# Kernel tuning notes

Hardware: AMD Instinct MI355X
Metric: run time of the kernel (lower is better)

## Reference

```python
import jax, jax.numpy as jnp
import numpy as np
from jax import lax

T, R, W, F_CWT, E, H, HG, NC, K = 16, 200, 50, 32, 128, 256, 256, 2, 20


def _make_wavelets():
    t = np.linspace(-1.0, 1.0, W)
    w0 = 6.0
    freqs = np.linspace(1.0, W / 2.0, F_CWT)
    wr = np.zeros((F_CWT, 1, W), np.float32)
    wi = np.zeros((F_CWT, 1, W), np.float32)
    for i, s in enumerate(freqs):
        norm = s ** (-0.5) * np.pi ** (-0.25)
        ts = t / s
        psi = norm * np.exp(1j * w0 * ts) * np.exp(-0.5 * ts ** 2)
        wr[i, 0] = psi.real.astype(np.float32)
        wi[i, 0] = psi.imag.astype(np.float32)
    return jnp.asarray(wr), jnp.asarray(wi)


def setup_inputs() -> dict:
    key = jax.random.key(0)
    ks = jax.random.split(key, 20)
    wr, wi = _make_wavelets()
    s = 0.05
    inp = {
        "time_windows": jax.random.normal(ks[0], (T, R, W), jnp.float32),
        "wav_real": wr, "wav_imag": wi,
        "conv1_w": jax.random.normal(ks[1], (16, 1, 3, 3), jnp.float32) * s,
        "conv1_b": jnp.zeros((16,), jnp.float32),
        "bn1_g": jnp.ones((16,), jnp.float32), "bn1_b": jnp.zeros((16,), jnp.float32),
        "conv2_w": jax.random.normal(ks[2], (32, 16, 3, 3), jnp.float32) * s,
        "conv2_b": jnp.zeros((32,), jnp.float32),
        "bn2_g": jnp.ones((32,), jnp.float32), "bn2_b": jnp.zeros((32,), jnp.float32),
        "fc_w": jax.random.normal(ks[3], (E, 32), jnp.float32) * s,
        "fc_b": jnp.zeros((E,), jnp.float32),
        "q_w": jax.random.normal(ks[4], (E, E), jnp.float32) * s,
        "q_b": jnp.zeros((E,), jnp.float32),
        "k_w": jax.random.normal(ks[5], (E, E), jnp.float32) * s,
        "k_b": jnp.zeros((E,), jnp.float32),
        "gcn1_w": jax.random.normal(ks[6], (E, H), jnp.float32) * s,
        "gcn1_b": jnp.zeros((H,), jnp.float32),
        "gcn2_w": jax.random.normal(ks[7], (H, H), jnp.float32) * s,
        "gcn2_b": jnp.zeros((H,), jnp.float32),
        "gru_wih": jax.random.normal(ks[8], (3 * HG, H), jnp.float32) * s,
        "gru_whh": jax.random.normal(ks[9], (3 * HG, HG), jnp.float32) * s,
        "gru_bih": jnp.zeros((3 * HG,), jnp.float32),
        "gru_bhh": jnp.zeros((3 * HG,), jnp.float32),
        "cls_w": jax.random.normal(ks[10], (NC, HG), jnp.float32) * s,
        "cls_b": jnp.zeros((NC,), jnp.float32),
    }
    return inp


def _conv_bn_relu_pool(x, w, b, g, beta):
    # conv2d k3 pad1, training-mode BN, relu, maxpool2 (floor)
    x = lax.conv_general_dilated(x, w, (1, 1), ((1, 1), (1, 1)),
                                 dimension_numbers=("NCHW", "OIHW", "NCHW"))
    x = x + b[None, :, None, None]
    mu = x.mean((0, 2, 3), keepdims=True)
    var = x.var((0, 2, 3), keepdims=True)
    x = (x - mu) * lax.rsqrt(var + 1e-5) * g[None, :, None, None] + beta[None, :, None, None]
    x = jax.nn.relu(x)
    return lax.reduce_window(x, -jnp.inf, lax.max, (1, 1, 2, 2), (1, 1, 2, 2), "VALID")


def _forward(time_windows, wav_real, wav_imag, conv1_w, conv1_b, bn1_g, bn1_b,
             conv2_w, conv2_b, bn2_g, bn2_b, fc_w, fc_b, q_w, q_b, k_w, k_b,
             gcn1_w, gcn1_b, gcn2_w, gcn2_b, gru_wih, gru_whh, gru_bih, gru_bhh,
             cls_w, cls_b):
    N = T * R
    x = time_windows.reshape(N, 1, W)
    pl = (W - 1) // 2
    pr = (W - 1) - pl  # torch padding='same' (extra on right)
    re = lax.conv_general_dilated(x, wav_real, (1,), [(pl, pr)],
                                  dimension_numbers=("NCH", "OIH", "NCH"))
    im = lax.conv_general_dilated(x, wav_imag, (1,), [(pl, pr)],
                                  dimension_numbers=("NCH", "OIH", "NCH"))
    scal = jnp.sqrt(re * re + im * im)              # [N, F_CWT, W]

    h = scal[:, None]                               # [N,1,F,W]
    h = _conv_bn_relu_pool(h, conv1_w, conv1_b, bn1_g, bn1_b)
    h = _conv_bn_relu_pool(h, conv2_w, conv2_b, bn2_g, bn2_b)
    pooled = h.mean((2, 3))                         # adaptive avg pool -> [N,32]
    emb = pooled @ fc_w.T + fc_b                    # [N,E]
    emb = emb.reshape(T, R, E)

    # sparse-attention graph generation (per window, vectorized over T)
    Q = emb @ q_w.T + q_b
    Kp = emb @ k_w.T + k_b
    attn = jnp.einsum("tre,tse->trs", Q, Kp) / (E ** 0.5)
    attn = jax.nn.leaky_relu(attn, 0.2)
    _, idx = lax.top_k(attn, K)                     # [T,R,K]
    mask = jnp.zeros_like(attn).at[
        jnp.arange(T)[:, None, None], jnp.arange(R)[None, :, None], idx].set(1.0)
    masked = attn * mask
    masked = jnp.where(masked == 0.0, -1e9, masked)
    adj = jax.nn.softmax(masked, axis=-1)           # [T,R,R] row-stochastic, topk-sparse

    # GCNConv x2 with edge weights (PyG gcn_norm: remaining self-loops weight 1,
    ii = jnp.arange(R)
    diag = adj[:, ii, ii]
    adj_sl = adj.at[:, ii, ii].set(jnp.where(diag == 0.0, 1.0, diag))
    Bm = jnp.swapaxes(adj_sl, 1, 2)
    deg = Bm.sum(-1)
    dinv = jnp.where(deg > 0, deg, 1.0) ** -0.5
    An = dinv[:, :, None] * Bm * dinv[:, None, :]   # [T,R,R]
    g = jax.nn.relu(jnp.einsum("trs,tsh->trh", An, emb @ gcn1_w) + gcn1_b)
    g = jax.nn.relu(jnp.einsum("trs,tsh->trh", An, g @ gcn2_w) + gcn2_b)
    g_emb = g.mean(1)                               # [T,H]

    # GRU over the T graph embeddings (batch 1, gate order r,z,n)
    def step(hprev, xt):
        gi = xt @ gru_wih.T + gru_bih
        gh = hprev @ gru_whh.T + gru_bhh
        ir, iz, inn = jnp.split(gi, 3)
        hr, hz, hn = jnp.split(gh, 3)
        r = jax.nn.sigmoid(ir + hr)
        z = jax.nn.sigmoid(iz + hz)
        n = jnp.tanh(inn + r * hn)
        return (1.0 - z) * n + z * hprev, None

    hT, _ = lax.scan(step, jnp.zeros((HG,), emb.dtype), g_emb)
    pred = (hT @ cls_w.T + cls_b)[None]             # [1,NC]

    edge_var = jnp.mean(jnp.var(adj, axis=0, ddof=1))
    avg_adj = adj.mean(0)[None]                     # [1,R,R]
    return pred, avg_adj, edge_var


def reference(time_windows, wav_real, wav_imag, conv1_w, conv1_b, bn1_g, bn1_b,
              conv2_w, conv2_b, bn2_g, bn2_b, fc_w, fc_b, q_w, q_b, k_w, k_b,
              gcn1_w, gcn1_b, gcn2_w, gcn2_b, gru_wih, gru_whh, gru_bih, gru_bhh,
              cls_w, cls_b):
    return _forward(time_windows, wav_real, wav_imag, conv1_w, conv1_b, bn1_g, bn1_b,
                    conv2_w, conv2_b, bn2_g, bn2_b, fc_w, fc_b, q_w, q_b, k_w, k_b,
                    gcn1_w, gcn1_b, gcn2_w, gcn2_b, gru_wih, gru_whh, gru_bih, gru_bhh,
                    cls_w, cls_b)
```

## Files before the change

### kernel.cpp

```cpp
#include <hip/hip_runtime.h>
#include <cfloat>
#include <cmath>

#define T_ 16
#define R_ 200
#define W_ 50
#define FCWT 32
#define E_ 128
#define K_ 20
#define N_ 3200
#define GRU_BLOCKS 6

__device__ __forceinline__ void waveReduce2(float& a, float& b) {
#pragma unroll
    for (int o = 32; o > 0; o >>= 1) {
        a += __shfl_down(a, o, 64);
        b += __shfl_down(b, o, 64);
    }
}

__global__ __launch_bounds__(256) void transpose_multi_kernel(const float* __restrict__ wih,
                                                              const float* __restrict__ whh,
                                                              const float* __restrict__ qw,
                                                              const float* __restrict__ kw,
                                                              const float* __restrict__ fcw,
                                                              float* __restrict__ wihT,
                                                              float* __restrict__ whhT,
                                                              float* __restrict__ qwT,
                                                              float* __restrict__ kwT,
                                                              float* __restrict__ fcwT) {
    int b = blockIdx.x, tid = threadIdx.x;
    if (b < 768) {
        int gid = b * 256 + tid; int k = gid / 768, j = gid % 768;
        wihT[gid] = wih[j * 256 + k];
    } else if (b < 1536) {
        int gid = (b - 768) * 256 + tid; int k = gid / 768, j = gid % 768;
        whhT[gid] = whh[j * 256 + k];
    } else if (b < 1600) {
        int gid = (b - 1536) * 256 + tid; int k = gid >> 7, e = gid & 127;
        qwT[gid] = qw[e * 128 + k];
    } else if (b < 1664) {
        int gid = (b - 1600) * 256 + tid; int k = gid >> 7, e = gid & 127;
        kwT[gid] = kw[e * 128 + k];
    } else {
        int gid = (b - 1664) * 256 + tid; int c = gid >> 7, e = gid & 127;
        fcwT[gid] = fcw[e * 32 + c];
    }
}

__global__ __launch_bounds__(256) void cwt_conv1_stats_kernel(const float* __restrict__ x,
                                                              const float* __restrict__ wr,
                                                              const float* __restrict__ wi,
                                                              const float* __restrict__ w1,
                                                              const float* __restrict__ b1,
                                                              float* __restrict__ scalP,
                                                              double* __restrict__ psum,
                                                              double* __restrict__ psq) {
    int n = blockIdx.x, tid = threadIdx.x;
    __shared__ float sxp[112];
    __shared__ float swr[FCWT * W_];
    __shared__ float swi[FCWT * W_];
    __shared__ float P1[34 * 52];
    __shared__ float ls[256], lq[256];
    if (tid < 112) sxp[tid] = (tid >= 24 && tid < 74) ? x[n * 50 + (tid - 24)] : 0.f;
    for (int idx = tid; idx < FCWT * W_; idx += 256) { swr[idx] = wr[idx]; swi[idx] = wi[idx]; }
    for (int idx = tid; idx < 34 * 52; idx += 256) P1[idx] = 0.f;
    __syncthreads();
    {
        int f = tid >> 3, cg = tid & 7, i0 = cg * 7;
        float xw[7], ar[7], ai[7];
#pragma unroll
        for (int d = 0; d < 7; ++d) { xw[d] = sxp[i0 + d]; ar[d] = 0.f; ai[d] = 0.f; }
        const float* wrf = &swr[f * 50];
        const float* wif = &swi[f * 50];
        for (int j = 0; j < 50; ++j) {
            float wrv = wrf[j], wiv = wif[j];
#pragma unroll
            for (int d = 0; d < 7; ++d) { ar[d] += xw[d] * wrv; ai[d] += xw[d] * wiv; }
#pragma unroll
            for (int d = 0; d < 6; ++d) xw[d] = xw[d + 1];
            xw[6] = sxp[i0 + j + 7];
        }
#pragma unroll
        for (int d = 0; d < 7; ++d) {
            int i = i0 + d;
            if (i < 50) P1[(f + 1) * 52 + i + 1] = sqrtf(ar[d] * ar[d] + ai[d] * ai[d]);
        }
    }
    __syncthreads();
    for (int idx = tid; idx < 34 * 52; idx += 256) scalP[(size_t)n * 1768 + idx] = P1[idx];
    int c = tid & 15, pg = tid >> 4;
    float wv[9];
#pragma unroll
    for (int k = 0; k < 9; ++k) wv[k] = w1[c * 9 + k];
    float bias = b1[c];
    const float* r0p = &P1[(2 * pg + 0) * 52];
    const float* r1p = &P1[(2 * pg + 1) * 52];
    const float* r2p = &P1[(2 * pg + 2) * 52];
    const float* r3p = &P1[(2 * pg + 3) * 52];
    float c0[4], c1[4];
    c0[0] = r0p[0]; c0[1] = r1p[0]; c0[2] = r2p[0]; c0[3] = r3p[0];
    c1[0] = r0p[1]; c1[1] = r1p[1]; c1[2] = r2p[1]; c1[3] = r3p[1];
    float s = 0.f, q = 0.f;
    for (int xx = 0; xx < 50; ++xx) {
        float c2[4];
        c2[0] = r0p[xx + 2]; c2[1] = r1p[xx + 2]; c2[2] = r2p[xx + 2]; c2[3] = r3p[xx + 2];
        float v0 = bias + c0[0] * wv[0] + c1[0] * wv[1] + c2[0] * wv[2]
                        + c0[1] * wv[3] + c1[1] * wv[4] + c2[1] * wv[5]
                        + c0[2] * wv[6] + c1[2] * wv[7] + c2[2] * wv[8];
        float v1 = bias + c0[1] * wv[0] + c1[1] * wv[1] + c2[1] * wv[2]
                        + c0[2] * wv[3] + c1[2] * wv[4] + c2[2] * wv[5]
                        + c0[3] * wv[6] + c1[3] * wv[7] + c2[3] * wv[8];
        s += v0 + v1; q += v0 * v0 + v1 * v1;
#pragma unroll
        for (int rr = 0; rr < 4; ++rr) { c0[rr] = c1[rr]; c1[rr] = c2[rr]; }
    }
    ls[tid] = s; lq[tid] = q;
    __syncthreads();
    if (tid < 16) {
        float ss = 0.f, qq = 0.f;
        for (int g = 0; g < 16; ++g) { ss += ls[tid + 16 * g]; qq += lq[tid + 16 * g]; }
        psum[n * 16 + tid] = (double)ss;
        psq[n * 16 + tid] = (double)qq;
    }
}

__global__ __launch_bounds__(256) void bn_finalize_kernel(const double* __restrict__ psum,
                                                          const double* __restrict__ psq,
                                                          const float* __restrict__ g,
                                                          const float* __restrict__ beta,
                                                          float* __restrict__ scale,
                                                          float* __restrict__ shift,
                                                          int C, double inv_count) {
    int c = blockIdx.x, tid = threadIdx.x;
    double s = 0.0, q = 0.0;
    for (int n = tid; n < N_; n += 256) { s += psum[n * C + c]; q += psq[n * C + c]; }
#pragma unroll
    for (int o = 32; o > 0; o >>= 1) { s += __shfl_down(s, o, 64); q += __shfl_down(q, o, 64); }
    __shared__ double sa[4], sb[4];
    int lane = tid & 63, wid = tid >> 6;
    if (lane == 0) { sa[wid] = s; sb[wid] = q; }
    __syncthreads();
    if (tid == 0) {
        s = sa[0] + sa[1] + sa[2] + sa[3];
        q = sb[0] + sb[1] + sb[2] + sb[3];
        double mu = s * inv_count;
        double var = q * inv_count - mu * mu;
        double rstd = 1.0 / sqrt(var + 1e-5);
        double gg = (double)g[c];
        scale[c] = (float)(gg * rstd);
        shift[c] = (float)((double)beta[c] - mu * rstd * gg);
    }
}

__global__ __launch_bounds__(256) void conv1_norm_pool_kernel(const float* __restrict__ scalP,
                                                              const float* __restrict__ w1,
                                                              const float* __restrict__ b1,
                                                              const float* __restrict__ scale,
                                                              const float* __restrict__ shift,
                                                              float* __restrict__ pooled1) {
    int n = blockIdx.x, tid = threadIdx.x;
    __shared__ float P1[34 * 52];
    __shared__ float outb[6400];
    for (int idx = tid; idx < 34 * 52; idx += 256) P1[idx] = scalP[(size_t)n * 1768 + idx];
    __syncthreads();
    int c = tid & 15, py = tid >> 4;
    float wv[9];
#pragma unroll
    for (int k = 0; k < 9; ++k) wv[k] = w1[c * 9 + k];
    float bias = b1[c], sc = scale[c], sh = shift[c];
    const float* r0p = &P1[(2 * py + 0) * 52];
    const float* r1p = &P1[(2 * py + 1) * 52];
    const float* r2p = &P1[(2 * py + 2) * 52];
    const float* r3p = &P1[(2 * py + 3) * 52];
    float c0[4], c1[4];
    c0[0] = r0p[0]; c0[1] = r1p[0]; c0[2] = r2p[0]; c0[3] = r3p[0];
    c1[0] = r0p[1]; c1[1] = r1p[1]; c1[2] = r2p[1]; c1[3] = r3p[1];
    float pmax = -FLT_MAX;
    for (int xx = 0; xx < 50; ++xx) {
        float c2[4];
        c2[0] = r0p[xx + 2]; c2[1] = r1p[xx + 2]; c2[2] = r2p[xx + 2]; c2[3] = r3p[xx + 2];
        float v0 = bias + c0[0] * wv[0] + c1[0] * wv[1] + c2[0] * wv[2]
                        + c0[1] * wv[3] + c1[1] * wv[4] + c2[1] * wv[5]
                        + c0[2] * wv[6] + c1[2] * wv[7] + c2[2] * wv[8];
        float v1 = bias + c0[1] * wv[0] + c1[1] * wv[1] + c2[1] * wv[2]
                        + c0[2] * wv[3] + c1[2] * wv[4] + c2[2] * wv[5]
                        + c0[3] * wv[6] + c1[3] * wv[7] + c2[3] * wv[8];
        float m2 = fmaxf(v0 * sc + sh, v1 * sc + sh);
        if ((xx & 1) == 0) pmax = m2;
        else outb[(c * 16 + py) * 25 + (xx >> 1)] = fmaxf(fmaxf(pmax, m2), 0.f);
#pragma unroll
        for (int rr = 0; rr < 4; ++rr) { c0[rr] = c1[rr]; c1[rr] = c2[rr]; }
    }
    __syncthreads();
    const float4* ob4 = (const float4*)outb;
    float4* p4 = (float4*)(pooled1 + (size_t)n * 6400);
    for (int idx = tid; idx < 1600; idx += 256) p4[idx] = ob4[idx];
}

__global__ __launch_bounds__(256) void conv2_compute_kernel(const float* __restrict__ pooled1,
                                                            const float* __restrict__ w2,
                                                            const float* __restrict__ b2,
                                                            float* __restrict__ mm,
                                                            double* __restrict__ psum,
                                                            double* __restrict__ psq) {
    int n = blockIdx.x, tid = threadIdx.x;
    __shared__ float P2[16 * 18 * 28];
    __shared__ float swT[144 * 32];
    __shared__ float ls[256], lq[256];
    for (int idx = tid; idx < 16 * 18 * 28; idx += 256) {
        int ci = idx / 504, rem = idx % 504, yy = rem / 28, xx = rem % 28;
        float v = 0.f;
        if (yy >= 1 && yy <= 16 && xx >= 1 && xx <= 25)
            v = pooled1[((size_t)n * 16 + ci) * 400 + (yy - 1) * 25 + (xx - 1)];
        P2[idx] = v;
    }
    for (int idx = tid; idx < 4608; idx += 256) {
        int co = idx / 144, r = idx % 144;
        swT[r * 32 + co] = w2[idx];
    }
    __syncthreads();
    int co = tid & 31, pg = tid >> 5;
    float bias = b2[co];
    float acc0[25], acc1[25];
#pragma unroll
    for (int cv = 0; cv < 25; ++cv) { acc0[cv] = bias; acc1[cv] = bias; }
    for (int ci = 0; ci < 16; ++ci) {
        const float* wb = &swT[ci * 288 + co];
        float w[9];
#pragma unroll
        for (int k = 0; k < 9; ++k) w[k] = wb[k * 32];
        const float* base = &P2[ci * 504 + (2 * pg) * 28];
#pragma unroll
        for (int iy = 0; iy < 4; ++iy) {
            float r[28];
            const float4* rp = (const float4*)(base + iy * 28);
#pragma unroll
            for (int m = 0; m < 7; ++m) {
                float4 v4 = rp[m];
                r[4 * m] = v4.x; r[4 * m + 1] = v4.y; r[4 * m + 2] = v4.z; r[4 * m + 3] = v4.w;
            }
            if (iy < 3) {
                int kb = iy * 3;
#pragma unroll
                for (int cv = 0; cv < 25; ++cv)
                    acc0[cv] += r[cv] * w[kb] + r[cv + 1] * w[kb + 1] + r[cv + 2] * w[kb + 2];
            }
            if (iy >= 1) {
                int kb = (iy - 1) * 3;
#pragma unroll
                for (int cv = 0; cv < 25; ++cv)
                    acc1[cv] += r[cv] * w[kb] + r[cv + 1] * w[kb + 1] + r[cv + 2] * w[kb + 2];
            }
        }
    }
    float s = 0.f, q = 0.f;
#pragma unroll
    for (int cv = 0; cv < 25; ++cv) {
        s += acc0[cv] + acc1[cv];
        q += acc0[cv] * acc0[cv] + acc1[cv] * acc1[cv];
    }
#pragma unroll
    for (int pc = 0; pc < 12; ++pc) {
        float v00 = acc0[2 * pc], v01 = acc0[2 * pc + 1];
        float v10 = acc1[2 * pc], v11 = acc1[2 * pc + 1];
        float mx = fmaxf(fmaxf(v00, v01), fmaxf(v10, v11));
        int cell = pg * 12 + pc;
        mm[((size_t)n * 96 + cell) * 32 + co] = mx;
    }
    ls[tid] = s; lq[tid] = q;
    __syncthreads();
    if (tid < 32) {
        float ss = 0.f, qq = 0.f;
        for (int g2 = 0; g2 < 8; ++g2) { ss += ls[tid + 32 * g2]; qq += lq[tid + 32 * g2]; }
        psum[n * 32 + tid] = (double)ss;
        psq[n * 32 + tid] = (double)qq;
    }
}

__global__ __launch_bounds__(256) void pm_fc_qk_kernel(const float* __restrict__ mm,
                                                       const float* __restrict__ scale,
                                                       const float* __restrict__ shift,
                                                       const float* __restrict__ fcwT,
                                                       const float* __restrict__ fc_b,
                                                       const float* __restrict__ qwT,
                                                       const float* __restrict__ q_b,
                                                       const float* __restrict__ kwT,
                                                       const float* __restrict__ k_b,
                                                       float* __restrict__ emb,
                                                       float* __restrict__ Q,
                                                       float* __restrict__ Kp) {
    int n = blockIdx.x, tid = threadIdx.x;
    int co = tid & 31, grp = tid >> 5;
    __shared__ float red[256];
    __shared__ float pm_s[32];
    __shared__ float se[128];
    float sc = scale[co], sh = shift[co];
    float acc = 0.f;
    for (int j = 0; j < 12; ++j) {
        int cell = grp * 12 + j;
        float mx = mm[((size_t)n * 96 + cell) * 32 + co];
        acc += fmaxf(mx * sc + sh, 0.f);
    }
    red[tid] = acc;
    __syncthreads();
    if (tid < 32) {
        float t = 0.f;
        for (int g = 0; g < 8; ++g) t += red[co + 32 * g];
        pm_s[tid] = t * (1.f / 96.f);
    }
    __syncthreads();
    if (tid < 128) {
        float a = fc_b[tid];
        for (int c = 0; c < 32; ++c) a += pm_s[c] * fcwT[c * 128 + tid];
        se[tid] = a;
        emb[(size_t)n * 128 + tid] = a;
    }
    __syncthreads();
    {
        int e = tid & 127, half = tid >> 7;
        const float* w = half ? kwT : qwT;
        float b = half ? k_b[e] : q_b[e];
        float a = b;
        for (int k = 0; k < 128; ++k) a += se[k] * w[k * 128 + e];
        if (half) Kp[(size_t)n * 128 + e] = a;
        else      Q[(size_t)n * 128 + e] = a;
    }
}

__global__ __launch_bounds__(256) void attn_topk_kernel(const float* __restrict__ Q,
                                                        const float* __restrict__ Kp,
                                                        float* __restrict__ adj) {
    int r = blockIdx.x, t = blockIdx.y, tid = threadIdx.x;
    __shared__ float sq[128];
    __shared__ float sc[200];
    if (tid < 128) sq[tid] = Q[(size_t)(t * 200 + r) * 128 + tid];
    __syncthreads();
    if (tid < 200) {
        const float4* kp4 = (const float4*)(Kp + (size_t)(t * 200 + tid) * 128);
        float acc = 0.f;
#pragma unroll 8
        for (int e4 = 0; e4 < 32; ++e4) {
            float4 k4 = kp4[e4];
            acc += sq[e4 * 4 + 0] * k4.x + sq[e4 * 4 + 1] * k4.y +
                   sq[e4 * 4 + 2] * k4.z + sq[e4 * 4 + 3] * k4.w;
        }
        acc = acc / 11.313708498984761f;
        sc[tid] = (acc >= 0.f) ? acc : 0.2f * acc;
    }
    __syncthreads();
    if (tid < 64) {
        int lane = tid;
        float v[4], w[4];
#pragma unroll
        for (int j = 0; j < 4; ++j) {
            int i = lane + 64 * j;
            float x = (i < 200) ? sc[i] : -FLT_MAX;
            v[j] = x; w[j] = x;
        }
        unsigned sel = 0;
        for (int it = 0; it < K_; ++it) {
            float best = -FLT_MAX; int bidx = 0x7fffffff;
#pragma unroll
            for (int j = 0; j < 4; ++j) {
                int i = lane + 64 * j;
                if (w[j] > best || (w[j] == best && i < bidx)) { best = w[j]; bidx = i; }
            }
#pragma unroll
            for (int off = 32; off > 0; off >>= 1) {
                float ob = __shfl_down(best, off, 64);
                int oi = __shfl_down(bidx, off, 64);
                if (ob > best || (ob == best && oi < bidx)) { best = ob; bidx = oi; }
            }
            bidx = __shfl(bidx, 0, 64);
            if ((bidx & 63) == lane) { int j = bidx >> 6; w[j] = -FLT_MAX; sel |= (1u << j); }
        }
        float mv[4]; float m = -FLT_MAX;
#pragma unroll
        for (int j = 0; j < 4; ++j) {
            int i = lane + 64 * j;
            float x = -1e9f;
            if (i < 200 && ((sel >> j) & 1u)) x = (v[j] == 0.f) ? -1e9f : v[j];
            mv[j] = x; m = fmaxf(m, x);
        }
#pragma unroll
        for (int off = 32; off > 0; off >>= 1) m = fmaxf(m, __shfl_xor(m, off, 64));
        float s = 0.f; float e[4];
#pragma unroll
        for (int j = 0; j < 4; ++j) {
            int i = lane + 64 * j;
            e[j] = (i < 200) ? expf(mv[j] - m) : 0.f;
            s += e[j];
        }
#pragma unroll
        for (int off = 32; off > 0; off >>= 1) s += __shfl_xor(s, off, 64);
        float inv = 1.f / s;
        size_t rowo = (size_t)(t * 200 + r) * 200;
#pragma unroll
        for (int j = 0; j < 4; ++j) {
            int i = lane + 64 * j;
            if (i < 200) adj[rowo + i] = e[j] * inv;
        }
    }
}

__global__ __launch_bounds__(256) void deg_kernel(const float* __restrict__ adj,
                                                  float* __restrict__ dinv) {
    int t = blockIdx.x, tid = threadIdx.x;
    if (tid < 200) {
        float acc = 0.f;
        for (int s = 0; s < 200; ++s) {
            float v = adj[(size_t)(t * 200 + s) * 200 + tid];
            if (s == tid) v = (v == 0.f) ? 1.f : v;
            acc += v;
        }
        float d = (acc > 0.f) ? acc : 1.f;
        dinv[t * 200 + tid] = 1.f / sqrtf(d);
    }
}

__global__ __launch_bounds__(256) void an_tile_kernel(const float* __restrict__ adj,
                                                      const float* __restrict__ dinv,
                                                      float* __restrict__ An) {
    int t = blockIdx.y;
    int tr = blockIdx.x >> 2, tc = blockIdx.x & 3;
    int r0 = tr * 50, s0 = tc * 50;
    int tid = threadIdx.x;
    __shared__ float Tt[50 * 51];
    __shared__ float dr[50], ds[50];
    for (int idx = tid; idx < 2500; idx += 256) {
        int a = idx / 50, b = idx % 50;
        Tt[a * 51 + b] = adj[(size_t)(t * 200 + s0 + a) * 200 + r0 + b];
    }
    if (tid < 50) dr[tid] = dinv[t * 200 + r0 + tid];
    else if (tid >= 64 && tid < 114) ds[tid - 64] = dinv[t * 200 + s0 + (tid - 64)];
    __syncthreads();
    for (int idx = tid; idx < 2500; idx += 256) {
        int rl = idx / 50, sl = idx % 50;
        float v = Tt[sl * 51 + rl];
        if (r0 + rl == s0 + sl) v = (v == 0.f) ? 1.f : v;
        An[(size_t)(t * 200 + r0 + rl) * 200 + s0 + sl] = dr[rl] * v * ds[sl];
    }
}

__global__ __launch_bounds__(256) void linear8_kernel(const float* __restrict__ in,
                                                      const float* __restrict__ w,
                                                      float* __restrict__ out, int IN) {
    int n0 = blockIdx.x * 8, h = threadIdx.x;
    __shared__ float sin_[8 * 256];
    for (int idx = h; idx < 8 * IN; idx += 256) sin_[idx] = in[(size_t)n0 * IN + idx];
    __syncthreads();
    float acc[8];
#pragma unroll
    for (int m = 0; m < 8; ++m) acc[m] = 0.f;
    for (int k = 0; k < IN; ++k) {
        float wv = w[k * 256 + h];
#pragma unroll
        for (int m = 0; m < 8; ++m) acc[m] += sin_[m * IN + k] * wv;
    }
#pragma unroll
    for (int m = 0; m < 8; ++m) out[(size_t)(n0 + m) * 256 + h] = acc[m];
}

__global__ __launch_bounds__(256) void gcn_agg_kernel(const float* __restrict__ An,
                                                      const float* __restrict__ X,
                                                      const float* __restrict__ b,
                                                      float* __restrict__ out) {
    int t = blockIdx.y, r0 = blockIdx.x * 8, h = threadIdx.x;
    __shared__ float sa[8 * 200];
    for (int idx = h; idx < 1600; idx += 256)
        sa[idx] = An[(size_t)(t * 200 + r0) * 200 + idx];
    __syncthreads();
    const float* Xt = X + (size_t)t * 200 * 256;
    float acc[8];
#pragma unroll
    for (int m = 0; m < 8; ++m) acc[m] = 0.f;
    for (int s = 0; s < 200; ++s) {
        float xv = Xt[s * 256 + h];
#pragma unroll
        for (int m = 0; m < 8; ++m) acc[m] += sa[m * 200 + s] * xv;
    }
    float bb = b[h];
#pragma unroll
    for (int m = 0; m < 8; ++m)
        out[(size_t)(t * 200 + r0 + m) * 256 + h] = fmaxf(acc[m] + bb, 0.f);
}

__global__ __launch_bounds__(256) void gemb_gi_kernel(const float* __restrict__ g2,
                                                      const float* __restrict__ wihT,
                                                      const float* __restrict__ bih,
                                                      float* __restrict__ GI) {
    int t = blockIdx.x, tid = threadIdx.x;
    __shared__ float sg[256];
    {
        float acc = 0.f;
        for (int r = 0; r < 200; ++r) acc += g2[(size_t)(t * 200 + r) * 256 + tid];
        sg[tid] = acc * (1.f / 200.f);
    }
    __syncthreads();
    for (int j = tid; j < 768; j += 256) {
        float acc = bih[j];
        for (int k = 0; k < 256; ++k) acc += sg[k] * wihT[k * 768 + j];
        GI[t * 768 + j] = acc;
    }
}

__global__ __launch_bounds__(256) void gru_cls_kernel(const float* __restrict__ GI,
                                                      const float* __restrict__ whhT,
                                                      const float* __restrict__ bhh,
                                                      const float* __restrict__ cls_w,
                                                      const float* __restrict__ cls_b,
                                                      float* __restrict__ GH,
                                                      int* __restrict__ flags,
                                                      float* __restrict__ out) {
    int b = blockIdx.x, tid = threadIdx.x;
    int jl = tid & 127;
    int kc = tid >> 7;
    int j = b * 128 + jl;
    float wreg[128];
#pragma unroll 16
    for (int k = 0; k < 128; ++k)
        wreg[k] = whhT[(size_t)(kc * 128 + k) * 768 + j];
    __shared__ float hcur[256];
    __shared__ float part[256];
    __shared__ float s0[4], s1[4];
    hcur[tid] = 0.f;
    __syncthreads();
    for (int st = 0; st < 16; ++st) {
        float p = 0.f;
        const float* hb = &hcur[kc * 128];
#pragma unroll 16
        for (int k = 0; k < 128; ++k) p += hb[k] * wreg[k];
        part[tid] = p;
        __syncthreads();
        if (tid < 128) {
            GH[st * 768 + b * 128 + tid] = part[tid] + part[tid + 128];
        }
        __threadfence();
        __syncthreads();
        if (tid == 0)
            __hip_atomic_store(&flags[b], st + 1, __ATOMIC_RELEASE, __HIP_MEMORY_SCOPE_AGENT);
        for (int bb = 0; bb < GRU_BLOCKS; ++bb) {
            while (__hip_atomic_load(&flags[bb], __ATOMIC_ACQUIRE, __HIP_MEMORY_SCOPE_AGENT) <= st)
                __builtin_amdgcn_s_sleep(2);
        }
        float ghr = GH[st * 768 + tid]       + bhh[tid];
        float ghz = GH[st * 768 + 256 + tid] + bhh[256 + tid];
        float ghn = GH[st * 768 + 512 + tid] + bhh[512 + tid];
        float gir = GI[st * 768 + tid];
        float giz = GI[st * 768 + 256 + tid];
        float gin = GI[st * 768 + 512 + tid];
        float r = 1.f / (1.f + expf(-(gir + ghr)));
        float z = 1.f / (1.f + expf(-(giz + ghz)));
        float nn = tanhf(gin + r * ghn);
        float hnew = (1.f - z) * nn + z * hcur[tid];
        __syncthreads();
        hcur[tid] = hnew;
        __syncthreads();
    }
    if (b == 0) {
        float v0 = hcur[tid] * cls_w[tid];
        float v1 = hcur[tid] * cls_w[256 + tid];
        waveReduce2(v0, v1);
        int lane = tid & 63, wid = tid >> 6;
        if (lane == 0) { s0[wid] = v0; s1[wid] = v1; }
        __syncthreads();
        if (tid == 0) {
            out[0] = s0[0] + s0[1] + s0[2] + s0[3] + cls_b[0];
            out[1] = s1[0] + s1[1] + s1[2] + s1[3] + cls_b[1];
        }
    }
}

__global__ __launch_bounds__(256) void edge_kernel(const float* __restrict__ adj,
                                                   float* __restrict__ out) {
    int gid = blockIdx.x * 256 + threadIdx.x;
    float var = 0.f;
    if (gid < 40000) {
        float v[16]; float s = 0.f;
#pragma unroll
        for (int t = 0; t < 16; ++t) { v[t] = adj[t * 40000 + gid]; s += v[t]; }
        float mean = s * (1.f / 16.f);
        float q = 0.f;
#pragma unroll
        for (int t = 0; t < 16; ++t) { float d = v[t] - mean; q += d * d; }
        var = q * (1.f / 15.f);
        out[2 + gid] = mean;
    }
    float dummy = 0.f;
    waveReduce2(var, dummy);
    __shared__ float sa[4];
    int lane = threadIdx.x & 63, wid = threadIdx.x >> 6;
    if (lane == 0) sa[wid] = var;
    __syncthreads();
    if (threadIdx.x == 0) {
        float bs = sa[0] + sa[1] + sa[2] + sa[3];
        atomicAdd(&out[40002], bs * (1.f / 40000.f));
    }
}

extern "C" void kernel_launch(void* const* d_in, const int* in_sizes, int n_in,
                              void* d_out, int out_size, void* d_ws, size_t ws_size,
                              hipStream_t stream) {
    const float* tw      = (const float*)d_in[0];
    const float* wav_r   = (const float*)d_in[1];
    const float* wav_i   = (const float*)d_in[2];
    const float* conv1_w = (const float*)d_in[3];
    const float* conv1_b = (const float*)d_in[4];
    const float* bn1_g   = (const float*)d_in[5];
    const float* bn1_b   = (const float*)d_in[6];
    const float* conv2_w = (const float*)d_in[7];
    const float* conv2_b = (const float*)d_in[8];
    const float* bn2_g   = (const float*)d_in[9];
    const float* bn2_b   = (const float*)d_in[10];
    const float* fc_w    = (const float*)d_in[11];
    const float* fc_b    = (const float*)d_in[12];
    const float* q_w     = (const float*)d_in[13];
    const float* q_b     = (const float*)d_in[14];
    const float* k_w     = (const float*)d_in[15];
    const float* k_b     = (const float*)d_in[16];
    const float* gcn1_w  = (const float*)d_in[17];
    const float* gcn1_b  = (const float*)d_in[18];
    const float* gcn2_w  = (const float*)d_in[19];
    const float* gcn2_b  = (const float*)d_in[20];
    const float* gru_wih = (const float*)d_in[21];
    const float* gru_whh = (const float*)d_in[22];
    const float* gru_bih = (const float*)d_in[23];
    const float* gru_bhh = (const float*)d_in[24];
    const float* cls_w   = (const float*)d_in[25];
    const float* cls_b   = (const float*)d_in[26];
    float* out = (float*)d_out;
    (void)in_sizes; (void)n_in; (void)out_size; (void)ws_size;

    const size_t POOLED1_B = (size_t)N_ * 6400 * 4;
    const size_t SCALU_B   = (size_t)N_ * 1768 * 4;
    const size_t MM_B      = (size_t)N_ * 96 * 32 * 4;
    const size_t P1S_B     = (size_t)N_ * 16 * 8;
    const size_t P2S_B     = (size_t)N_ * 32 * 8;
    const size_t WT_B      = (size_t)768 * 256 * 4;

    size_t off = 0;
    char* Wb = (char*)d_ws;
    auto take = [&](size_t bytes) -> char* {
        char* p = Wb + off;
        off += (bytes + 255) & ~(size_t)255;
        return p;
    };
    char*  pooled1U = take(POOLED1_B);
    char*  scalU    = take(SCALU_B);
    float* mm    = (float*)take(MM_B);
    double* p1sum = (double*)take(P1S_B);
    double* p1sq  = (double*)take(P1S_B);
    double* p2sum = (double*)take(P2S_B);
    double* p2sq  = (double*)take(P2S_B);
    float* scale1 = (float*)take(64 * 4);
    float* shift1 = (float*)take(64 * 4);
    float* scale2 = (float*)take(64 * 4);
    float* shift2 = (float*)take(64 * 4);
    float* wihT   = (float*)take(WT_B);
    float* whhT   = (float*)take(WT_B);
    float* qwT    = (float*)take(128 * 128 * 4);
    float* kwT    = (float*)take(128 * 128 * 4);
    float* fcwT   = (float*)take(32 * 128 * 4);
    float* dinv   = (float*)take((size_t)T_ * 200 * 4);
    float* GH     = (float*)take((size_t)16 * 768 * 4);
    int*   flags  = (int*)take(256);

    float* scalP = (float*)scalU;
    float* emb   = (float*)(scalU + 0);
    float* Q     = (float*)(scalU + 1638400);
    float* Kp    = (float*)(scalU + 2 * 1638400);

    float* pooled1 = (float*)pooled1U;
    size_t moff = 0;
    auto mtake = [&](size_t bytes) -> float* {
        float* p = (float*)(pooled1U + moff);
        moff += (bytes + 255) & ~(size_t)255;
        return p;
    };
    float* adj   = mtake((size_t)T_ * 200 * 200 * 4);
    float* An    = mtake((size_t)T_ * 200 * 200 * 4);
    float* X1    = mtake((size_t)N_ * 256 * 4);
    float* g1    = mtake((size_t)N_ * 256 * 4);
    float* X2    = mtake((size_t)N_ * 256 * 4);
    float* g2    = mtake((size_t)N_ * 256 * 4);
    float* GI    = mtake((size_t)T_ * 768 * 4);

    transpose_multi_kernel<<<1680, 256, 0, stream>>>(gru_wih, gru_whh, q_w, k_w, fc_w,
                                                     wihT, whhT, qwT, kwT, fcwT);
    cwt_conv1_stats_kernel<<<N_, 256, 0, stream>>>(tw, wav_r, wav_i, conv1_w, conv1_b,
                                                   scalP, p1sum, p1sq);
    bn_finalize_kernel<<<16, 256, 0, stream>>>(p1sum, p1sq, bn1_g, bn1_b, scale1, shift1,
                                               16, 1.0 / 5120000.0);
    conv1_norm_pool_kernel<<<N_, 256, 0, stream>>>(scalP, conv1_w, conv1_b, scale1, shift1,
                                                   pooled1);
    conv2_compute_kernel<<<N_, 256, 0, stream>>>(pooled1, conv2_w, conv2_b, mm,
                                                 p2sum, p2sq);
    bn_finalize_kernel<<<32, 256, 0, stream>>>(p2sum, p2sq, bn2_g, bn2_b, scale2, shift2,
                                               32, 1.0 / 1280000.0);
    pm_fc_qk_kernel<<<N_, 256, 0, stream>>>(mm, scale2, shift2, fcwT, fc_b,
                                            qwT, q_b, kwT, k_b, emb, Q, Kp);
    attn_topk_kernel<<<dim3(200, 16), 256, 0, stream>>>(Q, Kp, adj);
    deg_kernel<<<16, 256, 0, stream>>>(adj, dinv);
    an_tile_kernel<<<dim3(16, 16), 256, 0, stream>>>(adj, dinv, An);
    linear8_kernel<<<N_ / 8, 256, 0, stream>>>(emb, gcn1_w, X1, 128);
    gcn_agg_kernel<<<dim3(25, 16), 256, 0, stream>>>(An, X1, gcn1_b, g1);
    linear8_kernel<<<N_ / 8, 256, 0, stream>>>(g1, gcn2_w, X2, 256);
    gcn_agg_kernel<<<dim3(25, 16), 256, 0, stream>>>(An, X2, gcn2_b, g2);
    gemb_gi_kernel<<<16, 256, 0, stream>>>(g2, wihT, gru_bih, GI);
    hipMemsetAsync(flags, 0, 256, stream);
    gru_cls_kernel<<<GRU_BLOCKS, 256, 0, stream>>>(GI, whhT, gru_bhh, cls_w, cls_b,
                                                   GH, flags, out);
    hipMemsetAsync(out + 40002, 0, sizeof(float), stream);
    edge_kernel<<<(40000 + 255) / 256, 256, 0, stream>>>(adj, out);
}
```

Before: 878.5 us.

## Fuse conv1 pooling into CWT kernel, defer BN to conv2, widen GCN aggregation

The CWT kernel now max-pools the raw conv1 outputs and stores them, instead of writing the scalogram out and recomputing conv1 in a second kernel. BN1 scale/shift and ReLU are applied in conv2's load step, which relies on the BN scale being positive so that max-pool commutes with the affine map. The two memsets are folded into an extra transpose block, and GCN aggregation now computes 16 rows per block instead of 8. This removes a full kernel pass plus the scalogram round trip through memory, but the fused kernel uses more shared memory.

```diff
diff --git a/kernel.cpp b/kernel.cpp
--- a/kernel.cpp
+++ b/kernel.cpp
@@ -10,6 +10,7 @@
 #define K_ 20
 #define N_ 3200
 #define GRU_BLOCKS 6
+#define PW 53
 
 __device__ __forceinline__ void waveReduce2(float& a, float& b) {
 #pragma unroll
@@ -28,7 +29,9 @@
                                                               float* __restrict__ whhT,
                                                               float* __restrict__ qwT,
                                                               float* __restrict__ kwT,
-                                                              float* __restrict__ fcwT) {
+                                                              float* __restrict__ fcwT,
+                                                              int* __restrict__ flags,
+                                                              float* __restrict__ out) {
     int b = blockIdx.x, tid = threadIdx.x;
     if (b < 768) {
         int gid = b * 256 + tid; int k = gid / 768, j = gid % 768;
@@ -42,29 +45,33 @@
     } else if (b < 1664) {
         int gid = (b - 1600) * 256 + tid; int k = gid >> 7, e = gid & 127;
         kwT[gid] = kw[e * 128 + k];
-    } else {
+    } else if (b < 1680) {
         int gid = (b - 1664) * 256 + tid; int c = gid >> 7, e = gid & 127;
         fcwT[gid] = fcw[e * 32 + c];
-    }
-}
-
-__global__ __launch_bounds__(256) void cwt_conv1_stats_kernel(const float* __restrict__ x,
-                                                              const float* __restrict__ wr,
-                                                              const float* __restrict__ wi,
-                                                              const float* __restrict__ w1,
-                                                              const float* __restrict__ b1,
-                                                              float* __restrict__ scalP,
-                                                              double* __restrict__ psum,
-                                                              double* __restrict__ psq) {
+    } else {
+        if (tid < 64) flags[tid] = 0;
+        if (tid == 64) out[40002] = 0.f;
+    }
+}
+
+__global__ __launch_bounds__(256) void cwt_conv1_kernel(const float* __restrict__ x,
+                                                        const float* __restrict__ wr,
+                                                        const float* __restrict__ wi,
+                                                        const float* __restrict__ w1,
+                                                        const float* __restrict__ b1,
+                                                        float* __restrict__ pooled1max,
+                                                        double* __restrict__ psum,
+                                                        double* __restrict__ psq) {
     int n = blockIdx.x, tid = threadIdx.x;
     __shared__ float sxp[112];
     __shared__ float swr[FCWT * W_];
     __shared__ float swi[FCWT * W_];
-    __shared__ float P1[34 * 52];
+    __shared__ float P1[34 * PW];
     __shared__ float ls[256], lq[256];
+    __shared__ float outb[6400];
     if (tid < 112) sxp[tid] = (tid >= 24 && tid < 74) ? x[n * 50 + (tid - 24)] : 0.f;
     for (int idx = tid; idx < FCWT * W_; idx += 256) { swr[idx] = wr[idx]; swi[idx] = wi[idx]; }
-    for (int idx = tid; idx < 34 * 52; idx += 256) P1[idx] = 0.f;
+    for (int idx = tid; idx < 34 * PW; idx += 256) P1[idx] = 0.f;
     __syncthreads();
     {
         int f = tid >> 3, cg = tid & 7, i0 = cg * 7;
@@ -84,24 +91,23 @@
 #pragma unroll
         for (int d = 0; d < 7; ++d) {
             int i = i0 + d;
-            if (i < 50) P1[(f + 1) * 52 + i + 1] = sqrtf(ar[d] * ar[d] + ai[d] * ai[d]);
-        }
-    }
-    __syncthreads();
-    for (int idx = tid; idx < 34 * 52; idx += 256) scalP[(size_t)n * 1768 + idx] = P1[idx];
-    int c = tid & 15, pg = tid >> 4;
+            if (i < 50) P1[(f + 1) * PW + i + 1] = sqrtf(ar[d] * ar[d] + ai[d] * ai[d]);
+        }
+    }
+    __syncthreads();
+    int c = tid & 15, py = tid >> 4;
     float wv[9];
 #pragma unroll
     for (int k = 0; k < 9; ++k) wv[k] = w1[c * 9 + k];
     float bias = b1[c];
-    const float* r0p = &P1[(2 * pg + 0) * 52];
-    const float* r1p = &P1[(2 * pg + 1) * 52];
-    const float* r2p = &P1[(2 * pg + 2) * 52];
-    const float* r3p = &P1[(2 * pg + 3) * 52];
+    const float* r0p = &P1[(2 * py + 0) * PW];
+    const float* r1p = &P1[(2 * py + 1) * PW];
+    const float* r2p = &P1[(2 * py + 2) * PW];
+    const float* r3p = &P1[(2 * py + 3) * PW];
     float c0[4], c1[4];
     c0[0] = r0p[0]; c0[1] = r1p[0]; c0[2] = r2p[0]; c0[3] = r3p[0];
     c1[0] = r0p[1]; c1[1] = r1p[1]; c1[2] = r2p[1]; c1[3] = r3p[1];
-    float s = 0.f, q = 0.f;
+    float s = 0.f, q = 0.f, pmax = -FLT_MAX;
     for (int xx = 0; xx < 50; ++xx) {
         float c2[4];
         c2[0] = r0p[xx + 2]; c2[1] = r1p[xx + 2]; c2[2] = r2p[xx + 2]; c2[3] = r3p[xx + 2];
@@ -112,6 +118,9 @@
                         + c0[2] * wv[3] + c1[2] * wv[4] + c2[2] * wv[5]
                         + c0[3] * wv[6] + c1[3] * wv[7] + c2[3] * wv[8];
         s += v0 + v1; q += v0 * v0 + v1 * v1;
+        float m2 = fmaxf(v0, v1);
+        if ((xx & 1) == 0) pmax = m2;
+        else outb[(c * 16 + py) * 25 + (xx >> 1)] = fmaxf(pmax, m2);
 #pragma unroll
         for (int rr = 0; rr < 4; ++rr) { c0[rr] = c1[rr]; c1[rr] = c2[rr]; }
     }
@@ -123,6 +132,9 @@
         psum[n * 16 + tid] = (double)ss;
         psq[n * 16 + tid] = (double)qq;
     }
+    const float4* ob4 = (const float4*)outb;
+    float4* p4 = (float4*)(pooled1max + (size_t)n * 6400);
+    for (int idx = tid; idx < 1600; idx += 256) p4[idx] = ob4[idx];
 }
 
 __global__ __launch_bounds__(256) void bn_finalize_kernel(const double* __restrict__ psum,
@@ -153,52 +165,9 @@
     }
 }
 
-__global__ __launch_bounds__(256) void conv1_norm_pool_kernel(const float* __restrict__ scalP,
-                                                              const float* __restrict__ w1,
-                                                              const float* __restrict__ b1,
-                                                              const float* __restrict__ scale,
-                                                              const float* __restrict__ shift,
-                                                              float* __restrict__ pooled1) {
-    int n = blockIdx.x, tid = threadIdx.x;
-    __shared__ float P1[34 * 52];
-    __shared__ float outb[6400];
-    for (int idx = tid; idx < 34 * 52; idx += 256) P1[idx] = scalP[(size_t)n * 1768 + idx];
-    __syncthreads();
-    int c = tid & 15, py = tid >> 4;
-    float wv[9];
-#pragma unroll
-    for (int k = 0; k < 9; ++k) wv[k] = w1[c * 9 + k];
-    float bias = b1[c], sc = scale[c], sh = shift[c];
-    const float* r0p = &P1[(2 * py + 0) * 52];
-    const float* r1p = &P1[(2 * py + 1) * 52];
-    const float* r2p = &P1[(2 * py + 2) * 52];
-    const float* r3p = &P1[(2 * py + 3) * 52];
-    float c0[4], c1[4];
-    c0[0] = r0p[0]; c0[1] = r1p[0]; c0[2] = r2p[0]; c0[3] = r3p[0];
-    c1[0] = r0p[1]; c1[1] = r1p[1]; c1[2] = r2p[1]; c1[3] = r3p[1];
-    float pmax = -FLT_MAX;
-    for (int xx = 0; xx < 50; ++xx) {
-        float c2[4];
-        c2[0] = r0p[xx + 2]; c2[1] = r1p[xx + 2]; c2[2] = r2p[xx + 2]; c2[3] = r3p[xx + 2];
-        float v0 = bias + c0[0] * wv[0] + c1[0] * wv[1] + c2[0] * wv[2]
-                        + c0[1] * wv[3] + c1[1] * wv[4] + c2[1] * wv[5]
-                        + c0[2] * wv[6] + c1[2] * wv[7] + c2[2] * wv[8];
-        float v1 = bias + c0[1] * wv[0] + c1[1] * wv[1] + c2[1] * wv[2]
-                        + c0[2] * wv[3] + c1[2] * wv[4] + c2[2] * wv[5]
-                        + c0[3] * wv[6] + c1[3] * wv[7] + c2[3] * wv[8];
-        float m2 = fmaxf(v0 * sc + sh, v1 * sc + sh);
-        if ((xx & 1) == 0) pmax = m2;
-        else outb[(c * 16 + py) * 25 + (xx >> 1)] = fmaxf(fmaxf(pmax, m2), 0.f);
-#pragma unroll
-        for (int rr = 0; rr < 4; ++rr) { c0[rr] = c1[rr]; c1[rr] = c2[rr]; }
-    }
-    __syncthreads();
-    const float4* ob4 = (const float4*)outb;
-    float4* p4 = (float4*)(pooled1 + (size_t)n * 6400);
-    for (int idx = tid; idx < 1600; idx += 256) p4[idx] = ob4[idx];
-}
-
-__global__ __launch_bounds__(256) void conv2_compute_kernel(const float* __restrict__ pooled1,
+__global__ __launch_bounds__(256) void conv2_compute_kernel(const float* __restrict__ pooled1max,
+                                                            const float* __restrict__ scale1,
+                                                            const float* __restrict__ shift1,
                                                             const float* __restrict__ w2,
                                                             const float* __restrict__ b2,
                                                             float* __restrict__ mm,
@@ -211,8 +180,10 @@
     for (int idx = tid; idx < 16 * 18 * 28; idx += 256) {
         int ci = idx / 504, rem = idx % 504, yy = rem / 28, xx = rem % 28;
         float v = 0.f;
-        if (yy >= 1 && yy <= 16 && xx >= 1 && xx <= 25)
-            v = pooled1[((size_t)n * 16 + ci) * 400 + (yy - 1) * 25 + (xx - 1)];
+        if (yy >= 1 && yy <= 16 && xx >= 1 && xx <= 25) {
+            float raw = pooled1max[((size_t)n * 16 + ci) * 400 + (yy - 1) * 25 + (xx - 1)];
+            v = fmaxf(raw * scale1[ci] + shift1[ci], 0.f);
+        }
         P2[idx] = v;
     }
     for (int idx = tid; idx < 4608; idx += 256) {
@@ -462,27 +433,27 @@
     for (int m = 0; m < 8; ++m) out[(size_t)(n0 + m) * 256 + h] = acc[m];
 }
 
-__global__ __launch_bounds__(256) void gcn_agg_kernel(const float* __restrict__ An,
-                                                      const float* __restrict__ X,
-                                                      const float* __restrict__ b,
-                                                      float* __restrict__ out) {
-    int t = blockIdx.y, r0 = blockIdx.x * 8, h = threadIdx.x;
-    __shared__ float sa[8 * 200];
-    for (int idx = h; idx < 1600; idx += 256)
-        sa[idx] = An[(size_t)(t * 200 + r0) * 200 + idx];
+__global__ __launch_bounds__(256) void gcn_agg16_kernel(const float* __restrict__ An,
+                                                        const float* __restrict__ X,
+                                                        const float* __restrict__ b,
+                                                        float* __restrict__ out) {
+    int t = blockIdx.y, r0 = blockIdx.x * 16, h = threadIdx.x;
+    __shared__ float sa[16 * 200];
+    int rows = (200 - r0 < 16) ? (200 - r0) : 16;
+    for (int idx = h; idx < 3200; idx += 256)
+        sa[idx] = (idx < rows * 200) ? An[(size_t)(t * 200 + r0) * 200 + idx] : 0.f;
     __syncthreads();
     const float* Xt = X + (size_t)t * 200 * 256;
-    float acc[8];
-#pragma unroll
-    for (int m = 0; m < 8; ++m) acc[m] = 0.f;
+    float acc[16];
+#pragma unroll
+    for (int m = 0; m < 16; ++m) acc[m] = 0.f;
     for (int s = 0; s < 200; ++s) {
         float xv = Xt[s * 256 + h];
 #pragma unroll
-        for (int m = 0; m < 8; ++m) acc[m] += sa[m * 200 + s] * xv;
+        for (int m = 0; m < 16; ++m) acc[m] += sa[m * 200 + s] * xv;
     }
     float bb = b[h];
-#pragma unroll
-    for (int m = 0; m < 8; ++m)
+    for (int m = 0; m < rows; ++m)
         out[(size_t)(t * 200 + r0 + m) * 256 + h] = fmaxf(acc[m] + bb, 0.f);
 }
 
@@ -633,7 +604,6 @@
     (void)in_sizes; (void)n_in; (void)out_size; (void)ws_size;
 
     const size_t POOLED1_B = (size_t)N_ * 6400 * 4;
-    const size_t SCALU_B   = (size_t)N_ * 1768 * 4;
     const size_t MM_B      = (size_t)N_ * 96 * 32 * 4;
     const size_t P1S_B     = (size_t)N_ * 16 * 8;
     const size_t P2S_B     = (size_t)N_ * 32 * 8;
@@ -647,7 +617,6 @@
         return p;
     };
     char*  pooled1U = take(POOLED1_B);
-    char*  scalU    = take(SCALU_B);
     float* mm    = (float*)take(MM_B);
     double* p1sum = (double*)take(P1S_B);
     double* p1sq  = (double*)take(P1S_B);
@@ -665,11 +634,9 @@
     float* dinv   = (float*)take((size_t)T_ * 200 * 4);
     float* GH     = (float*)take((size_t)16 * 768 * 4);
     int*   flags  = (int*)take(256);
-
-    float* scalP = (float*)scalU;
-    float* emb   = (float*)(scalU + 0);
-    float* Q     = (float*)(scalU + 1638400);
-    float* Kp    = (float*)(scalU + 2 * 1638400);
+    float* emb    = (float*)take((size_t)N_ * 128 * 4);
+    float* Q      = (float*)take((size_t)N_ * 128 * 4);
+    float* Kp     = (float*)take((size_t)N_ * 128 * 4);
 
     float* pooled1 = (float*)pooled1U;
     size_t moff = 0;
@@ -686,16 +653,15 @@
     float* g2    = mtake((size_t)N_ * 256 * 4);
     float* GI    = mtake((size_t)T_ * 768 * 4);
 
-    transpose_multi_kernel<<<1680, 256, 0, stream>>>(gru_wih, gru_whh, q_w, k_w, fc_w,
-                                                     wihT, whhT, qwT, kwT, fcwT);
-    cwt_conv1_stats_kernel<<<N_, 256, 0, stream>>>(tw, wav_r, wav_i, conv1_w, conv1_b,
-                                                   scalP, p1sum, p1sq);
+    transpose_multi_kernel<<<1681, 256, 0, stream>>>(gru_wih, gru_whh, q_w, k_w, fc_w,
+                                                     wihT, whhT, qwT, kwT, fcwT,
+                                                     flags, out);
+    cwt_conv1_kernel<<<N_, 256, 0, stream>>>(tw, wav_r, wav_i, conv1_w, conv1_b,
+                                             pooled1, p1sum, p1sq);
     bn_finalize_kernel<<<16, 256, 0, stream>>>(p1sum, p1sq, bn1_g, bn1_b, scale1, shift1,
                                                16, 1.0 / 5120000.0);
-    conv1_norm_pool_kernel<<<N_, 256, 0, stream>>>(scalP, conv1_w, conv1_b, scale1, shift1,
-                                                   pooled1);
-    conv2_compute_kernel<<<N_, 256, 0, stream>>>(pooled1, conv2_w, conv2_b, mm,
-                                                 p2sum, p2sq);
+    conv2_compute_kernel<<<N_, 256, 0, stream>>>(pooled1, scale1, shift1, conv2_w, conv2_b,
+                                                 mm, p2sum, p2sq);
     bn_finalize_kernel<<<32, 256, 0, stream>>>(p2sum, p2sq, bn2_g, bn2_b, scale2, shift2,
                                                32, 1.0 / 1280000.0);
     pm_fc_qk_kernel<<<N_, 256, 0, stream>>>(mm, scale2, shift2, fcwT, fc_b,
@@ -704,13 +670,11 @@
     deg_kernel<<<16, 256, 0, stream>>>(adj, dinv);
     an_tile_kernel<<<dim3(16, 16), 256, 0, stream>>>(adj, dinv, An);
     linear8_kernel<<<N_ / 8, 256, 0, stream>>>(emb, gcn1_w, X1, 128);
-    gcn_agg_kernel<<<dim3(25, 16), 256, 0, stream>>>(An, X1, gcn1_b, g1);
+    gcn_agg16_kernel<<<dim3(13, 16), 256, 0, stream>>>(An, X1, gcn1_b, g1);
     linear8_kernel<<<N_ / 8, 256, 0, stream>>>(g1, gcn2_w, X2, 256);
-    gcn_agg_kernel<<<dim3(25, 16), 256, 0, stream>>>(An, X2, gcn2_b, g2);
+    gcn_agg16_kernel<<<dim3(13, 16), 256, 0, stream>>>(An, X2, gcn2_b, g2);
     gemb_gi_kernel<<<16, 256, 0, stream>>>(g2, wihT, gru_bih, GI);
-    hipMemsetAsync(flags, 0, 256, stream);
     gru_cls_kernel<<<GRU_BLOCKS, 256, 0, stream>>>(GI, whhT, gru_bhh, cls_w, cls_b,
                                                    GH, flags, out);
-    hipMemsetAsync(out + 40002, 0, sizeof(float), stream);
     edge_kernel<<<(40000 + 255) / 256, 256, 0, stream>>>(adj, out);
 }
```

New measurement: 880.3 us. About the same (+0.2%).
